# Kernel optimization log

Hardware: AMD Instinct MI355X
Metric: run time of the kernel (lower is better)

Reference implementation:

```python
import jax, jax.numpy as jnp
import numpy as np

HEADS = 8
DIM_HEAD = 64
SCALE = DIM_HEAD ** -0.5


def setup_inputs() -> dict:
    key = jax.random.key(0)
    k1, k2, k3 = jax.random.split(key, 3)
    b, dim, n = 4, 256, 2048
    hidden = HEADS * DIM_HEAD  # 512
    x = jax.random.normal(k1, (b, dim, n), dtype=jnp.float32)
    # Conv1d kernel-size-1 weights are pointwise linear maps over channels.
    w_qkv = jax.random.normal(k2, (3 * hidden, dim), dtype=jnp.float32) * (dim ** -0.5)
    w_out = jax.random.normal(k3, (dim, hidden), dtype=jnp.float32) * (hidden ** -0.5)
    b_out = jnp.zeros((dim,), dtype=jnp.float32)
    return {"x": x, "w_qkv": w_qkv, "w_out": w_out, "b_out": b_out}


def reference(x, w_qkv, w_out, b_out):
    b, dim, n = x.shape
    hidden = w_out.shape[1]
    # pointwise conv1d == channel matmul: [3h, dim] x [b, dim, n] -> [b, 3h, n]
    qkv = jnp.einsum('oi,bin->bon', w_qkv, x)
    q, k, v = jnp.split(qkv, 3, axis=1)
    # b (h c) n -> b h c n
    reshape = lambda t: t.reshape(b, HEADS, DIM_HEAD, n)
    q, k, v = reshape(q) * SCALE, reshape(k), reshape(v)
    sim = jnp.einsum('bhdi,bhdj->bhij', q, k)          # [b, h, n, n]
    attn = jax.nn.softmax(sim, axis=-1)
    out = jnp.einsum('bhij,bhdj->bhid', attn, v)        # [b, h, n, d]
    # b h n d -> b (h d) n
    out = out.transpose(0, 1, 3, 2).reshape(b, hidden, n)
    return jnp.einsum('oi,bin->bon', w_out, out) + b_out[None, :, None]
```

## Files before the change

kernel.cpp:

```cpp
#include <hip/hip_runtime.h>
#include <stdint.h>

#define SEQ  2048
#define DIMC 256
#define HID  512
#define NH   8
#define DH   64

typedef __attribute__((ext_vector_type(8))) short bf16x8;
typedef __attribute__((ext_vector_type(4))) float f32x4;
typedef __attribute__((ext_vector_type(16))) float f32x16;
typedef __attribute__((ext_vector_type(2))) unsigned uint2v;
typedef __attribute__((address_space(1))) const uint32_t guint_t;
typedef __attribute__((address_space(3))) uint32_t luint_t;

__device__ __forceinline__ void gld16(const void* g, void* l) {
  __builtin_amdgcn_global_load_lds((guint_t*)g, (luint_t*)l, 16, 0, 0);
}

__device__ __forceinline__ void barrier_raw() {
  asm volatile("" ::: "memory");
  __builtin_amdgcn_s_barrier();
  asm volatile("" ::: "memory");
}
#define WAITVM(n) asm volatile("s_waitcnt vmcnt(" #n ")" ::: "memory")

__device__ __forceinline__ unsigned short f2bf(float f) {
  union { float f; uint32_t u; } v; v.f = f;
  return (unsigned short)((v.u + 0x7FFFu + ((v.u >> 16) & 1u)) >> 16);
}

__device__ __forceinline__ uint32_t fbits(float f) {
  union { float f; uint32_t u; } v; v.f = f; return v.u;
}
__device__ __forceinline__ float ffrombits(uint32_t u) {
  union { uint32_t u; float f; } v; v.u = u; return v.f;
}

__device__ __forceinline__ uint32_t cvtpk(float a, float b) {
  uint32_t r;
  asm("v_cvt_pk_bf16_f32 %0, %1, %2" : "=v"(r) : "v"(a), "v"(b));
  return r;
}

__device__ __forceinline__ void swap32(uint32_t& a, uint32_t& b) {
#if __has_builtin(__builtin_amdgcn_permlane32_swap)
  uint2v r = __builtin_amdgcn_permlane32_swap(a, b, false, false);
  a = r[0]; b = r[1];
#else
  uint32_t aw = __shfl_xor(a, 32);
  uint32_t bw = __shfl_xor(b, 32);
  bool lo = (threadIdx.x & 32) == 0;
  uint32_t an = lo ? a : bw;
  uint32_t bn = lo ? aw : b;
  a = an; b = bn;
#endif
}

__global__ __launch_bounds__(256) void prep_kernel(
    const float* __restrict__ x, const float* __restrict__ wqkv,
    const float* __restrict__ wout,
    unsigned short* __restrict__ wqkv_b, unsigned short* __restrict__ wout_b,
    unsigned short* __restrict__ xT) {
  __shared__ float tile[64][65];
  int blk = blockIdx.x;
  int t = threadIdx.x;
  if (blk < 384) {
    int idx = blk * 1024 + t * 4;
    float4 v = *(const float4*)(wqkv + idx);
    float s = ((idx >> 8) < HID) ? 0.18033688011112042f : 1.0f;
    ushort4 o;
    o.x = f2bf(v.x * s); o.y = f2bf(v.y * s);
    o.z = f2bf(v.z * s); o.w = f2bf(v.w * s);
    *(ushort4*)(wqkv_b + idx) = o;
    return;
  }
  if (blk < 512) {
    int idx = (blk - 384) * 1024 + t * 4;
    float4 v = *(const float4*)(wout + idx);
    ushort4 o;
    o.x = f2bf(v.x); o.y = f2bf(v.y); o.z = f2bf(v.z); o.w = f2bf(v.w);
    *(ushort4*)(wout_b + idx) = o;
    return;
  }
  int tid = blk - 512;
  int b  = tid >> 7;
  int r  = tid & 127;
  int i0 = (r >> 5) * 64;
  int n0 = (r & 31) * 64;
  const float* xb = x + (size_t)b * DIMC * SEQ;
  int tn = t & 15, ti = t >> 4;
#pragma unroll
  for (int j = 0; j < 4; j++) {
    int il = ti + j * 16;
    float4 v = *(const float4*)(xb + (size_t)(i0 + il) * SEQ + n0 + tn * 4);
    tile[il][tn*4+0] = v.x; tile[il][tn*4+1] = v.y;
    tile[il][tn*4+2] = v.z; tile[il][tn*4+3] = v.w;
  }
  __syncthreads();
  unsigned short* xTb = xT + (size_t)b * SEQ * DIMC;
#pragma unroll
  for (int j = 0; j < 4; j++) {
    int nl = ti + j * 16;
    int i4 = tn * 4;
    uint2 pk;
    pk.x = (uint32_t)f2bf(tile[i4+0][nl]) | ((uint32_t)f2bf(tile[i4+1][nl]) << 16);
    pk.y = (uint32_t)f2bf(tile[i4+2][nl]) | ((uint32_t)f2bf(tile[i4+3][nl]) << 16);
    *(uint2*)(xTb + (size_t)(n0 + nl) * DIMC + i0 + i4) = pk;
  }
}

__global__ __launch_bounds__(256, 3) void qkv_gemm(
    const unsigned short* __restrict__ wq, const unsigned short* __restrict__ xT,
    unsigned short* __restrict__ Qs, unsigned short* __restrict__ Ks,
    unsigned short* __restrict__ Vt) {
  __shared__ unsigned short lds[32768];
  int id = blockIdx.x + 12 * blockIdx.y + 192 * blockIdx.z;
  int xcd = id & 7, wg = id >> 3;
  int pair = xcd * 8 + wg / 12;
  int o0 = (wg % 12) * 128;
  int n0 = (pair & 15) * 128;
  int b  = pair >> 4;
  int t  = threadIdx.x;
  int wv = t >> 6, l = t & 63, l15 = l & 15, q = l >> 4;
  int wm = (wv & 1) * 64, wn = (wv >> 1) * 64;
  f32x4 acc[4][4];
#pragma unroll
  for (int i = 0; i < 4; i++)
#pragma unroll
    for (int j = 0; j < 4; j++) acc[i][j] = (f32x4){0.f, 0.f, 0.f, 0.f};
  const unsigned short* Ag = wq + (size_t)o0 * DIMC;
  const unsigned short* Bg = xT + ((size_t)b * SEQ + n0) * DIMC;
  int lrow8 = l >> 3, lcol = l & 7;

  auto stage = [&](int kk, int buf) {
    unsigned short* la = lds + (buf << 14);
    unsigned short* lb = la + 8192;
    int k0 = kk * 64;
#pragma unroll
    for (int c0 = 0; c0 < 4; c0++) {
      int c = wv * 4 + c0;
      int row = c * 8 + lrow8;
      int sg = lcol ^ (row & 7);
      gld16(Ag + (size_t)row * DIMC + k0 + sg * 8, la + c * 512);
      gld16(Bg + (size_t)row * DIMC + k0 + sg * 8, lb + c * 512);
    }
  };

  stage(0, 0);
  for (int kk = 0; kk < 4; kk++) {
    int cur = kk & 1;
    WAITVM(0);
    barrier_raw();
    if (kk < 3) stage(kk + 1, cur ^ 1);
    unsigned short* la = lds + (cur << 14);
    unsigned short* lb = la + 8192;
#pragma unroll
    for (int kh = 0; kh < 2; kh++) {
      bf16x8 af[4], bfr[4];
#pragma unroll
      for (int mt = 0; mt < 4; mt++) {
        int row = wm + mt*16 + l15;
        af[mt] = *(const bf16x8*)(la + row*64 + ((kh*4 + q) ^ (row & 7)) * 8);
      }
#pragma unroll
      for (int nt = 0; nt < 4; nt++) {
        int row = wn + nt*16 + l15;
        bfr[nt] = *(const bf16x8*)(lb + row*64 + ((kh*4 + q) ^ (row & 7)) * 8);
      }
#pragma unroll
      for (int mt = 0; mt < 4; mt++)
#pragma unroll
        for (int nt = 0; nt < 4; nt++)
          acc[mt][nt] = __builtin_amdgcn_mfma_f32_16x16x32_bf16(af[mt], bfr[nt], acc[mt][nt], 0, 0, 0);
    }
  }
  barrier_raw();
  int seg3 = o0 >> 9;
  int h0   = (o0 & 511) >> 6;
  if (seg3 == 2) {
#pragma unroll
    for (int mt = 0; mt < 4; mt++)
#pragma unroll
      for (int nt = 0; nt < 4; nt++)
#pragma unroll
        for (int r = 0; r < 4; r++) {
          int ol = wm + mt * 16 + q * 4 + r;
          int nn = wn + nt * 16 + l15;
          lds[ol * 136 + nn] = f2bf(acc[mt][nt][r]);
        }
    __syncthreads();
#pragma unroll
    for (int i = 0; i < 8; i++) {
      int idx = i * 256 + t;
      int ol  = idx >> 4;
      int nnb = (idx & 15) * 8;
      uint4 v = *(const uint4*)(lds + ol * 136 + nnb);
      int h = h0 + (ol >> 6), d = ol & 63;
      *(uint4*)(Vt + (((size_t)b * NH + h) * DH + d) * SEQ + n0 + nnb) = v;
    }
  } else {
    unsigned short* dst = (seg3 == 0) ? Qs : Ks;
#pragma unroll
    for (int mt = 0; mt < 4; mt++)
#pragma unroll
      for (int nt = 0; nt < 4; nt++)
#pragma unroll
        for (int r = 0; r < 4; r++) {
          int ol = wm + mt * 16 + q * 4 + r;
          int nn = wn + nt * 16 + l15;
          lds[nn * 136 + ol] = f2bf(acc[mt][nt][r]);
        }
    __syncthreads();
#pragma unroll
    for (int i = 0; i < 8; i++) {
      int idx = i * 256 + t;
      int nn  = idx >> 4;
      int olb = (idx & 15) * 8;
      uint4 v = *(const uint4*)(lds + nn * 136 + olb);
      int h = h0 + (olb >> 6), d = olb & 63;
      *(uint4*)(dst + (((size_t)b * NH + h) * SEQ + n0 + nn) * DH + d) = v;
    }
  }
}

__global__ __launch_bounds__(256, 4) void attn_kernel(
    const unsigned short* __restrict__ Qs, const unsigned short* __restrict__ Ks,
    const unsigned short* __restrict__ Vt, unsigned short* __restrict__ AO) {
  __shared__ unsigned short KVs[16384];
  __shared__ float Lc[128];
  int id = blockIdx.x;
  int s  = id >> 3;
  int bh = (id & 7) * 4 + (s & 3);
  int q0 = (s >> 2) * 64;
  int b = bh >> 3, h = bh & 7;
  int t = threadIdx.x;
  int w = t >> 6, l = t & 63, l31 = l & 31, lh = l >> 5;
  int cg = w & 1, qg = w >> 1;
  const unsigned short* Qg = Qs + ((size_t)bh * SEQ + q0 + qg * 32) * DH;
  bf16x8 qb[4];
#pragma unroll
  for (int kc = 0; kc < 4; kc++)
    qb[kc] = *(const bf16x8*)(Qg + l31 * DH + kc*16 + lh*8);
  f32x16 oacc[2];
  float lsum = 0.f;
#pragma unroll
  for (int dt = 0; dt < 2; dt++)
#pragma unroll
    for (int r = 0; r < 16; r++) oacc[dt][r] = 0.f;

  const unsigned short* Ksrc = Ks + ((size_t)bh * SEQ + cg * 1024) * DH;
  const unsigned short* Vsrc = Vt + (size_t)bh * DH * SEQ + cg * 1024;

  const unsigned short* sgp[4];
  unsigned short* dst0;
  size_t step;
  if (w < 2) {
#pragma unroll
    for (int g = 0; g < 4; g++) {
      int kr = g * 8 + (l >> 3);
      sgp[g] = Ksrc + (size_t)kr * DH + ((l & 7) ^ (kr & 7)) * 8;
    }
    dst0 = (unsigned short*)KVs + cg * 2048;
    step = (size_t)32 * DH;
  } else {
#pragma unroll
    for (int g = 0; g < 4; g++) {
      int r = g * 8 + (l >> 3);
      int u = (l & 7) ^ (r & 7);
      int d = (u >> 2) * 32 + r;
      int j = u & 3;
      sgp[g] = Vsrc + (size_t)d * SEQ + j * 8;
    }
    dst0 = (unsigned short*)KVs + 4096 + cg * 2048;
    step = 32;
  }

  auto stage = [&](int it2, int buf) {
    size_t off = (size_t)it2 * step;
    unsigned short* dstb = dst0 + buf * 8192;
#pragma unroll
    for (int g = 0; g < 4; g++)
      gld16(sgp[g] + off, dstb + g * 512);
  };

  stage(0, 0);
  for (int it = 0; it < 32; it++) {
    int cur = it & 1;
    WAITVM(0);
    barrier_raw();
    if (it < 31) stage(it + 1, cur ^ 1);
    const unsigned short* Kst = KVs + cur * 8192 + cg * 2048;
    const unsigned short* Vst = KVs + cur * 8192 + 4096 + cg * 2048;
    f32x16 st;
#pragma unroll
    for (int r = 0; r < 16; r++) st[r] = 0.f;
    __builtin_amdgcn_s_setprio(1);
#pragma unroll
    for (int kc = 0; kc < 4; kc++) {
      bf16x8 kf = *(const bf16x8*)(Kst + l31 * 64 + ((kc*2 + lh) ^ (l31 & 7)) * 8);
      st = __builtin_amdgcn_mfma_f32_32x32x16_bf16(kf, qb[kc], st, 0, 0, 0);
    }
    __builtin_amdgcn_s_setprio(0);
    bf16x8 vf[2][2];
#pragma unroll
    for (int kc2 = 0; kc2 < 2; kc2++)
#pragma unroll
      for (int dt = 0; dt < 2; dt++)
        vf[kc2][dt] = *(const bf16x8*)(Vst + l31 * 64 +
                                       ((dt*4 + kc2*2 + lh) ^ (l31 & 7)) * 8);
    float p[16];
#pragma unroll
    for (int r = 0; r < 16; r++) p[r] = __builtin_amdgcn_exp2f(st[r]);
    {
      float t0 = p[0]+p[1],  t1 = p[2]+p[3],  t2 = p[4]+p[5],  t3 = p[6]+p[7];
      float t4 = p[8]+p[9],  t5 = p[10]+p[11], t6 = p[12]+p[13], t7 = p[14]+p[15];
      float u0 = t0+t1, u1 = t2+t3, u2 = t4+t5, u3 = t6+t7;
      lsum += (u0+u1) + (u2+u3);
    }
    bf16x8 af[2];
#pragma unroll
    for (int hf = 0; hf < 2; hf++) {
      uint32_t xs[4], ys[4];
#pragma unroll
      for (int j = 0; j < 4; j++) {
        xs[j] = fbits(p[hf*8 + j]);
        ys[j] = fbits(p[hf*8 + 4 + j]);
        swap32(xs[j], ys[j]);
      }
      union { uint32_t u[4]; bf16x8 v; } cv;
      cv.u[0] = cvtpk(ffrombits(xs[0]), ffrombits(xs[1]));
      cv.u[1] = cvtpk(ffrombits(xs[2]), ffrombits(xs[3]));
      cv.u[2] = cvtpk(ffrombits(ys[0]), ffrombits(ys[1]));
      cv.u[3] = cvtpk(ffrombits(ys[2]), ffrombits(ys[3]));
      af[hf] = cv.v;
    }
    __builtin_amdgcn_s_setprio(1);
#pragma unroll
    for (int kc2 = 0; kc2 < 2; kc2++)
#pragma unroll
      for (int dt = 0; dt < 2; dt++)
        oacc[dt] = __builtin_amdgcn_mfma_f32_32x32x16_bf16(af[kc2], vf[kc2][dt], oacc[dt], 0, 0, 0);
    __builtin_amdgcn_s_setprio(0);
  }
  {
    float v = lsum;
    v += __shfl_xor(v, 32);
    if (l < 32) Lc[cg * 64 + qg * 32 + l31] = v;
  }
  __syncthreads();
  float* Oc = (float*)KVs;
  if (cg == 1) {
#pragma unroll
    for (int dt = 0; dt < 2; dt++)
#pragma unroll
      for (int r = 0; r < 16; r++) {
        int qrow = qg*32 + (r & 3) + 8*(r >> 2) + 4*lh;
        Oc[qrow * 64 + dt*32 + l31] = oacc[dt][r];
      }
  }
  __syncthreads();
  if (cg == 0) {
    unsigned short* AOb = AO + (size_t)b * SEQ * HID + h * DH;
#pragma unroll
    for (int r = 0; r < 16; r++) {
      int qrow = qg*32 + (r & 3) + 8*(r >> 2) + 4*lh;
      float inv = __builtin_amdgcn_rcpf(Lc[qrow] + Lc[64 + qrow]);
      int n = q0 + qrow;
#pragma unroll
      for (int dt = 0; dt < 2; dt++) {
        float val = (oacc[dt][r] + Oc[qrow * 64 + dt*32 + l31]) * inv;
        AOb[(size_t)n * HID + dt*32 + l31] = f2bf(val);
      }
    }
  }
}

__global__ __launch_bounds__(256, 2) void out_gemm(
    const unsigned short* __restrict__ wo, const unsigned short* __restrict__ AO,
    const float* __restrict__ bias, float* __restrict__ out) {
  __shared__ unsigned short lds[16384];
  int id = blockIdx.x + 4 * blockIdx.y + 128 * blockIdx.z;
  int xcd = id & 7, wg = id >> 3;
  int pair = xcd * 16 + (wg >> 2);
  int o0 = (wg & 3) * 64;
  int n0 = (pair & 31) * 64;
  int b  = pair >> 5;
  int t  = threadIdx.x;
  int wv = t >> 6, l = t & 63, l15 = l & 15, q = l >> 4;
  int wm = (wv & 1) * 32, wn = (wv >> 1) * 32;
  f32x4 acc[2][2];
#pragma unroll
  for (int i = 0; i < 2; i++)
#pragma unroll
    for (int j = 0; j < 2; j++) acc[i][j] = (f32x4){0.f,0.f,0.f,0.f};
  const unsigned short* Ag = wo + (size_t)o0 * HID;
  const unsigned short* Bg = AO + ((size_t)b * SEQ + n0) * HID;
  int lrow8 = l >> 3, lcol = l & 7;

  auto stage = [&](int kk, int buf) {
    unsigned short* la = lds + buf * 8192;
    unsigned short* lb = la + 4096;
    int k0 = kk * 64;
#pragma unroll
    for (int c0 = 0; c0 < 2; c0++) {
      int c = wv * 2 + c0;
      int row = c * 8 + lrow8;
      int sg = lcol ^ (row & 7);
      gld16(Ag + (size_t)row * HID + k0 + sg * 8, la + c * 512);
      gld16(Bg + (size_t)row * HID + k0 + sg * 8, lb + c * 512);
    }
  };

  stage(0, 0);
  for (int kk = 0; kk < 8; kk++) {
    int cur = kk & 1;
    WAITVM(0);
    barrier_raw();
    if (kk < 7) stage(kk + 1, cur ^ 1);
    unsigned short* la = lds + cur * 8192;
    unsigned short* lb = la + 4096;
#pragma unroll
    for (int kh = 0; kh < 2; kh++) {
      bf16x8 af[2], bfr[2];
#pragma unroll
      for (int mt = 0; mt < 2; mt++) {
        int row = wm + mt*16 + l15;
        af[mt] = *(const bf16x8*)(la + row*64 + ((kh*4 + q) ^ (row & 7)) * 8);
      }
#pragma unroll
      for (int nt = 0; nt < 2; nt++) {
        int row = wn + nt*16 + l15;
        bfr[nt] = *(const bf16x8*)(lb + row*64 + ((kh*4 + q) ^ (row & 7)) * 8);
      }
#pragma unroll
      for (int mt = 0; mt < 2; mt++)
#pragma unroll
        for (int nt = 0; nt < 2; nt++)
          acc[mt][nt] = __builtin_amdgcn_mfma_f32_16x16x32_bf16(af[mt], bfr[nt], acc[mt][nt], 0,0,0);
    }
  }
#pragma unroll
  for (int mt = 0; mt < 2; mt++)
#pragma unroll
    for (int nt = 0; nt < 2; nt++)
#pragma unroll
      for (int r = 0; r < 4; r++) {
        int o2 = o0 + wm + mt*16 + q*4 + r;
        int n  = n0 + wn + nt*16 + l15;
        out[((size_t)b * DIMC + o2) * SEQ + n] = acc[mt][nt][r] + bias[o2];
      }
}

extern "C" void kernel_launch(void* const* d_in, const int* in_sizes, int n_in,
                              void* d_out, int out_size, void* d_ws, size_t ws_size,
                              hipStream_t stream) {
  const float* x    = (const float*)d_in[0];
  const float* wqkv = (const float*)d_in[1];
  const float* wout = (const float*)d_in[2];
  const float* bout = (const float*)d_in[3];
  float* out = (float*)d_out;
  char* ws = (char*)d_ws;
  unsigned short* wqkv_b = (unsigned short*)(ws);
  unsigned short* wout_b = (unsigned short*)(ws + 786432);
  unsigned short* xT     = (unsigned short*)(ws + 1048576);
  unsigned short* Qs     = (unsigned short*)(ws + 5242880);
  unsigned short* Ks     = (unsigned short*)(ws + 13631488);
  unsigned short* Vt     = (unsigned short*)(ws + 22020096);
  unsigned short* AO     = (unsigned short*)(ws + 30408704);
  prep_kernel<<<1024, 256, 0, stream>>>(x, wqkv, wout, wqkv_b, wout_b, xT);
  qkv_gemm<<<dim3(12, 16, 4), 256, 0, stream>>>(wqkv_b, xT, Qs, Ks, Vt);
  attn_kernel<<<1024, 256, 0, stream>>>(Qs, Ks, Vt, AO);
  out_gemm<<<dim3(4, 32, 4), 256, 0, stream>>>(wout_b, AO, bout, out);
}
```

Before: 137.3 us.

## Split attention keys across four waves with per-wave private K/V pipelines

Each wave now handles all 64 query rows (two 32-row tiles) over its own quarter of the key sequence, so each K fragment read from LDS feeds two MFMAs. Each wave stages its own K and V tiles into private double buffers using vmcnt-based waits instead of block-wide barriers inside the loop. The four partial outputs and row sums are reduced through LDS at the end. LDS per block doubles and launch bounds drop to 2 blocks per SU, which lowers occupancy and adds a larger final reduction.

Result: slower. 144.7 us (+5.4%).

```diff
diff --git a/kernel.cpp b/kernel.cpp
--- a/kernel.cpp
+++ b/kernel.cpp
@@ -224,11 +224,11 @@
   }
 }
 
-__global__ __launch_bounds__(256, 4) void attn_kernel(
+__global__ __launch_bounds__(256, 2) void attn_kernel(
     const unsigned short* __restrict__ Qs, const unsigned short* __restrict__ Ks,
     const unsigned short* __restrict__ Vt, unsigned short* __restrict__ AO) {
-  __shared__ unsigned short KVs[16384];
-  __shared__ float Lc[128];
+  __shared__ unsigned short KVs[32768];
+  __shared__ float Lc[256];
   int id = blockIdx.x;
   int s  = id >> 3;
   int bh = (id & 7) * 4 + (s & 3);
@@ -236,70 +236,62 @@
   int b = bh >> 3, h = bh & 7;
   int t = threadIdx.x;
   int w = t >> 6, l = t & 63, l31 = l & 31, lh = l >> 5;
-  int cg = w & 1, qg = w >> 1;
-  const unsigned short* Qg = Qs + ((size_t)bh * SEQ + q0 + qg * 32) * DH;
-  bf16x8 qb[4];
-#pragma unroll
-  for (int kc = 0; kc < 4; kc++)
-    qb[kc] = *(const bf16x8*)(Qg + l31 * DH + kc*16 + lh*8);
-  f32x16 oacc[2];
-  float lsum = 0.f;
-#pragma unroll
-  for (int dt = 0; dt < 2; dt++)
-#pragma unroll
-    for (int r = 0; r < 16; r++) oacc[dt][r] = 0.f;
-
-  const unsigned short* Ksrc = Ks + ((size_t)bh * SEQ + cg * 1024) * DH;
-  const unsigned short* Vsrc = Vt + (size_t)bh * DH * SEQ + cg * 1024;
-
-  const unsigned short* sgp[4];
-  unsigned short* dst0;
-  size_t step;
-  if (w < 2) {
+
+  const unsigned short* Qg = Qs + ((size_t)bh * SEQ + q0) * DH;
+  bf16x8 qb[2][4];
+#pragma unroll
+  for (int qt = 0; qt < 2; qt++)
+#pragma unroll
+    for (int kc = 0; kc < 4; kc++)
+      qb[qt][kc] = *(const bf16x8*)(Qg + (qt*32 + l31) * DH + kc*16 + lh*8);
+
+  f32x16 oacc[2][2];
+  float lsum0 = 0.f, lsum1 = 0.f;
+#pragma unroll
+  for (int qt = 0; qt < 2; qt++)
+#pragma unroll
+    for (int dt = 0; dt < 2; dt++)
+#pragma unroll
+      for (int r = 0; r < 16; r++) oacc[qt][dt][r] = 0.f;
+
+  const unsigned short* Ksrc = Ks + ((size_t)bh * SEQ + w * 512) * DH;
+  const unsigned short* Vsrc = Vt + (size_t)bh * DH * SEQ + w * 512;
+  int l3 = l >> 3, l7 = l & 7;
+  int u  = l7 ^ (l3 & 7);
+  const unsigned short* Kg0 = Ksrc + (size_t)l3 * DH + u * 8;
+  const unsigned short* Vg0 = Vsrc + (size_t)((u >> 2) * 32 + l3) * SEQ + (u & 3) * 8;
+  unsigned short* myK = (unsigned short*)KVs + w * 8192;
+
+  auto stage = [&](int it2, int buf) {
+    const unsigned short* kp = Kg0 + (size_t)it2 * 32 * DH;
+    const unsigned short* vp = Vg0 + it2 * 32;
+    unsigned short* kd = myK + buf * 4096;
+    unsigned short* vd = kd + 2048;
 #pragma unroll
     for (int g = 0; g < 4; g++) {
-      int kr = g * 8 + (l >> 3);
-      sgp[g] = Ksrc + (size_t)kr * DH + ((l & 7) ^ (kr & 7)) * 8;
-    }
-    dst0 = (unsigned short*)KVs + cg * 2048;
-    step = (size_t)32 * DH;
-  } else {
-#pragma unroll
-    for (int g = 0; g < 4; g++) {
-      int r = g * 8 + (l >> 3);
-      int u = (l & 7) ^ (r & 7);
-      int d = (u >> 2) * 32 + r;
-      int j = u & 3;
-      sgp[g] = Vsrc + (size_t)d * SEQ + j * 8;
-    }
-    dst0 = (unsigned short*)KVs + 4096 + cg * 2048;
-    step = 32;
-  }
-
-  auto stage = [&](int it2, int buf) {
-    size_t off = (size_t)it2 * step;
-    unsigned short* dstb = dst0 + buf * 8192;
-#pragma unroll
-    for (int g = 0; g < 4; g++)
-      gld16(sgp[g] + off, dstb + g * 512);
+      gld16(kp + g * 8 * DH, kd + g * 512);
+      gld16(vp + (size_t)g * 8 * SEQ, vd + g * 512);
+    }
   };
 
   stage(0, 0);
-  for (int it = 0; it < 32; it++) {
-    int cur = it & 1;
-    WAITVM(0);
-    barrier_raw();
-    if (it < 31) stage(it + 1, cur ^ 1);
-    const unsigned short* Kst = KVs + cur * 8192 + cg * 2048;
-    const unsigned short* Vst = KVs + cur * 8192 + 4096 + cg * 2048;
-    f32x16 st;
-#pragma unroll
-    for (int r = 0; r < 16; r++) st[r] = 0.f;
+  stage(1, 1);
+  for (int it = 0; it < 16; it++) {
+    int buf = it & 1;
+    if (it == 15) { WAITVM(0); } else { WAITVM(8); }
+    const unsigned short* Kst = myK + buf * 4096;
+    const unsigned short* Vst = Kst + 2048;
+    f32x16 st[2];
+#pragma unroll
+    for (int qt = 0; qt < 2; qt++)
+#pragma unroll
+      for (int r = 0; r < 16; r++) st[qt][r] = 0.f;
     __builtin_amdgcn_s_setprio(1);
 #pragma unroll
     for (int kc = 0; kc < 4; kc++) {
       bf16x8 kf = *(const bf16x8*)(Kst + l31 * 64 + ((kc*2 + lh) ^ (l31 & 7)) * 8);
-      st = __builtin_amdgcn_mfma_f32_32x32x16_bf16(kf, qb[kc], st, 0, 0, 0);
+      st[0] = __builtin_amdgcn_mfma_f32_32x32x16_bf16(kf, qb[0][kc], st[0], 0, 0, 0);
+      st[1] = __builtin_amdgcn_mfma_f32_32x32x16_bf16(kf, qb[1][kc], st[1], 0, 0, 0);
     }
     __builtin_amdgcn_s_setprio(0);
     bf16x8 vf[2][2];
@@ -309,70 +301,82 @@
       for (int dt = 0; dt < 2; dt++)
         vf[kc2][dt] = *(const bf16x8*)(Vst + l31 * 64 +
                                        ((dt*4 + kc2*2 + lh) ^ (l31 & 7)) * 8);
-    float p[16];
-#pragma unroll
-    for (int r = 0; r < 16; r++) p[r] = __builtin_amdgcn_exp2f(st[r]);
-    {
-      float t0 = p[0]+p[1],  t1 = p[2]+p[3],  t2 = p[4]+p[5],  t3 = p[6]+p[7];
-      float t4 = p[8]+p[9],  t5 = p[10]+p[11], t6 = p[12]+p[13], t7 = p[14]+p[15];
-      float u0 = t0+t1, u1 = t2+t3, u2 = t4+t5, u3 = t6+t7;
-      lsum += (u0+u1) + (u2+u3);
-    }
-    bf16x8 af[2];
-#pragma unroll
-    for (int hf = 0; hf < 2; hf++) {
-      uint32_t xs[4], ys[4];
-#pragma unroll
-      for (int j = 0; j < 4; j++) {
-        xs[j] = fbits(p[hf*8 + j]);
-        ys[j] = fbits(p[hf*8 + 4 + j]);
-        swap32(xs[j], ys[j]);
-      }
-      union { uint32_t u[4]; bf16x8 v; } cv;
-      cv.u[0] = cvtpk(ffrombits(xs[0]), ffrombits(xs[1]));
-      cv.u[1] = cvtpk(ffrombits(xs[2]), ffrombits(xs[3]));
-      cv.u[2] = cvtpk(ffrombits(ys[0]), ffrombits(ys[1]));
-      cv.u[3] = cvtpk(ffrombits(ys[2]), ffrombits(ys[3]));
-      af[hf] = cv.v;
-    }
-    __builtin_amdgcn_s_setprio(1);
-#pragma unroll
-    for (int kc2 = 0; kc2 < 2; kc2++)
+#pragma unroll
+    for (int qt = 0; qt < 2; qt++) {
+      float p[16];
+#pragma unroll
+      for (int r = 0; r < 16; r++) p[r] = __builtin_amdgcn_exp2f(st[qt][r]);
+      {
+        float t0=p[0]+p[1],  t1=p[2]+p[3],  t2=p[4]+p[5],   t3=p[6]+p[7];
+        float t4=p[8]+p[9],  t5=p[10]+p[11], t6=p[12]+p[13], t7=p[14]+p[15];
+        float a = ((t0+t1)+(t2+t3)) + ((t4+t5)+(t6+t7));
+        if (qt == 0) lsum0 += a; else lsum1 += a;
+      }
+      bf16x8 af[2];
+#pragma unroll
+      for (int hf = 0; hf < 2; hf++) {
+        uint32_t xs[4], ys[4];
+#pragma unroll
+        for (int j = 0; j < 4; j++) {
+          xs[j] = fbits(p[hf*8 + j]);
+          ys[j] = fbits(p[hf*8 + 4 + j]);
+          swap32(xs[j], ys[j]);
+        }
+        union { uint32_t u[4]; bf16x8 v; } cv;
+        cv.u[0] = cvtpk(ffrombits(xs[0]), ffrombits(xs[1]));
+        cv.u[1] = cvtpk(ffrombits(xs[2]), ffrombits(xs[3]));
+        cv.u[2] = cvtpk(ffrombits(ys[0]), ffrombits(ys[1]));
+        cv.u[3] = cvtpk(ffrombits(ys[2]), ffrombits(ys[3]));
+        af[hf] = cv.v;
+      }
+      __builtin_amdgcn_s_setprio(1);
+#pragma unroll
+      for (int kc2 = 0; kc2 < 2; kc2++)
+#pragma unroll
+        for (int dt = 0; dt < 2; dt++)
+          oacc[qt][dt] = __builtin_amdgcn_mfma_f32_32x32x16_bf16(af[kc2], vf[kc2][dt], oacc[qt][dt], 0, 0, 0);
+      __builtin_amdgcn_s_setprio(0);
+    }
+    if (it < 14) {
+      asm volatile("s_waitcnt lgkmcnt(0)" ::: "memory");
+      stage(it + 2, buf);
+    }
+  }
+  lsum0 += __shfl_xor(lsum0, 32);
+  lsum1 += __shfl_xor(lsum1, 32);
+  if (l < 32) { Lc[w*64 + l31] = lsum0; Lc[w*64 + 32 + l31] = lsum1; }
+  __syncthreads();
+  float* Ob = (float*)KVs;
+  if (w > 0) {
+    float* Ow = Ob + (w - 1) * 4096;
+#pragma unroll
+    for (int qt = 0; qt < 2; qt++)
 #pragma unroll
       for (int dt = 0; dt < 2; dt++)
-        oacc[dt] = __builtin_amdgcn_mfma_f32_32x32x16_bf16(af[kc2], vf[kc2][dt], oacc[dt], 0, 0, 0);
-    __builtin_amdgcn_s_setprio(0);
-  }
-  {
-    float v = lsum;
-    v += __shfl_xor(v, 32);
-    if (l < 32) Lc[cg * 64 + qg * 32 + l31] = v;
+#pragma unroll
+        for (int r = 0; r < 16; r++) {
+          int qrow = qt*32 + (r & 3) + 8*(r >> 2) + 4*lh;
+          Ow[qrow * 64 + dt*32 + l31] = oacc[qt][dt][r];
+        }
   }
   __syncthreads();
-  float* Oc = (float*)KVs;
-  if (cg == 1) {
-#pragma unroll
-    for (int dt = 0; dt < 2; dt++)
+  if (w == 0) {
+    unsigned short* AOb = AO + (size_t)b * SEQ * HID + h * DH;
+#pragma unroll
+    for (int qt = 0; qt < 2; qt++)
 #pragma unroll
       for (int r = 0; r < 16; r++) {
-        int qrow = qg*32 + (r & 3) + 8*(r >> 2) + 4*lh;
-        Oc[qrow * 64 + dt*32 + l31] = oacc[dt][r];
-      }
-  }
-  __syncthreads();
-  if (cg == 0) {
-    unsigned short* AOb = AO + (size_t)b * SEQ * HID + h * DH;
-#pragma unroll
-    for (int r = 0; r < 16; r++) {
-      int qrow = qg*32 + (r & 3) + 8*(r >> 2) + 4*lh;
-      float inv = __builtin_amdgcn_rcpf(Lc[qrow] + Lc[64 + qrow]);
-      int n = q0 + qrow;
-#pragma unroll
-      for (int dt = 0; dt < 2; dt++) {
-        float val = (oacc[dt][r] + Oc[qrow * 64 + dt*32 + l31]) * inv;
-        AOb[(size_t)n * HID + dt*32 + l31] = f2bf(val);
-      }
-    }
+        int qrow = qt*32 + (r & 3) + 8*(r >> 2) + 4*lh;
+        float inv = __builtin_amdgcn_rcpf(Lc[qrow] + Lc[64 + qrow] +
+                                          Lc[128 + qrow] + Lc[192 + qrow]);
+        int n = q0 + qrow;
+#pragma unroll
+        for (int dt = 0; dt < 2; dt++) {
+          int idx = qrow * 64 + dt*32 + l31;
+          float val = (oacc[qt][dt][r] + Ob[idx] + Ob[4096 + idx] + Ob[8192 + idx]) * inv;
+          AOb[(size_t)n * HID + dt*32 + l31] = f2bf(val);
+        }
+      }
   }
 }
 
```

## Double attention query tile per block so more waves share K/V staging

Applied to the files above, without the earlier changes.

The attention kernel now runs 512-thread blocks, each covering 128 queries instead of 64, with half as many blocks. Each staged K/V tile in LDS is reused by four query groups instead of two, which halves global K/V traffic per query. The load work is split across eight waves, and the row-sum and partial-output reduction buffers are resized. The launch bound of 512 threads with 4 blocks per CU caps per-thread registers more tightly, which could cause spills. Only 512 blocks are launched, so the grid fills the device less evenly.

Measured after the change: 130.1 us. -5.2%, faster.

```diff
diff --git a/kernel.cpp b/kernel.cpp
--- a/kernel.cpp
+++ b/kernel.cpp
@@ -224,15 +224,15 @@
   }
 }
 
-__global__ __launch_bounds__(256, 4) void attn_kernel(
+__global__ __launch_bounds__(512, 4) void attn_kernel(
     const unsigned short* __restrict__ Qs, const unsigned short* __restrict__ Ks,
     const unsigned short* __restrict__ Vt, unsigned short* __restrict__ AO) {
   __shared__ unsigned short KVs[16384];
-  __shared__ float Lc[128];
+  __shared__ float Lc[256];
   int id = blockIdx.x;
   int s  = id >> 3;
   int bh = (id & 7) * 4 + (s & 3);
-  int q0 = (s >> 2) * 64;
+  int q0 = (s >> 2) * 128;
   int b = bh >> 3, h = bh & 7;
   int t = threadIdx.x;
   int w = t >> 6, l = t & 63, l31 = l & 31, lh = l >> 5;
@@ -249,39 +249,40 @@
 #pragma unroll
     for (int r = 0; r < 16; r++) oacc[dt][r] = 0.f;
 
-  const unsigned short* Ksrc = Ks + ((size_t)bh * SEQ + cg * 1024) * DH;
-  const unsigned short* Vsrc = Vt + (size_t)bh * DH * SEQ + cg * 1024;
-
-  const unsigned short* sgp[4];
+  int which = w >> 1, half = w & 1;
+  const unsigned short* sgp[2];
   unsigned short* dst0;
   size_t step;
-  if (w < 2) {
-#pragma unroll
-    for (int g = 0; g < 4; g++) {
+  if (which < 2) {
+    const unsigned short* Ksrc = Ks + ((size_t)bh * SEQ + which * 1024) * DH;
+#pragma unroll
+    for (int gi = 0; gi < 2; gi++) {
+      int g = half * 2 + gi;
       int kr = g * 8 + (l >> 3);
-      sgp[g] = Ksrc + (size_t)kr * DH + ((l & 7) ^ (kr & 7)) * 8;
-    }
-    dst0 = (unsigned short*)KVs + cg * 2048;
+      sgp[gi] = Ksrc + (size_t)kr * DH + ((l & 7) ^ (kr & 7)) * 8;
+    }
+    dst0 = (unsigned short*)KVs + which * 2048 + half * 1024;
     step = (size_t)32 * DH;
   } else {
-#pragma unroll
-    for (int g = 0; g < 4; g++) {
+    const unsigned short* Vsrc = Vt + (size_t)bh * DH * SEQ + (which - 2) * 1024;
+#pragma unroll
+    for (int gi = 0; gi < 2; gi++) {
+      int g = half * 2 + gi;
       int r = g * 8 + (l >> 3);
       int u = (l & 7) ^ (r & 7);
       int d = (u >> 2) * 32 + r;
       int j = u & 3;
-      sgp[g] = Vsrc + (size_t)d * SEQ + j * 8;
-    }
-    dst0 = (unsigned short*)KVs + 4096 + cg * 2048;
+      sgp[gi] = Vsrc + (size_t)d * SEQ + j * 8;
+    }
+    dst0 = (unsigned short*)KVs + 4096 + (which - 2) * 2048 + half * 1024;
     step = 32;
   }
 
   auto stage = [&](int it2, int buf) {
     size_t off = (size_t)it2 * step;
     unsigned short* dstb = dst0 + buf * 8192;
-#pragma unroll
-    for (int g = 0; g < 4; g++)
-      gld16(sgp[g] + off, dstb + g * 512);
+    gld16(sgp[0] + off, dstb);
+    gld16(sgp[1] + off, dstb + 512);
   };
 
   stage(0, 0);
@@ -313,10 +314,9 @@
 #pragma unroll
     for (int r = 0; r < 16; r++) p[r] = __builtin_amdgcn_exp2f(st[r]);
     {
-      float t0 = p[0]+p[1],  t1 = p[2]+p[3],  t2 = p[4]+p[5],  t3 = p[6]+p[7];
-      float t4 = p[8]+p[9],  t5 = p[10]+p[11], t6 = p[12]+p[13], t7 = p[14]+p[15];
-      float u0 = t0+t1, u1 = t2+t3, u2 = t4+t5, u3 = t6+t7;
-      lsum += (u0+u1) + (u2+u3);
+      float t0=p[0]+p[1],  t1=p[2]+p[3],  t2=p[4]+p[5],   t3=p[6]+p[7];
+      float t4=p[8]+p[9],  t5=p[10]+p[11], t6=p[12]+p[13], t7=p[14]+p[15];
+      lsum += ((t0+t1)+(t2+t3)) + ((t4+t5)+(t6+t7));
     }
     bf16x8 af[2];
 #pragma unroll
@@ -346,7 +346,7 @@
   {
     float v = lsum;
     v += __shfl_xor(v, 32);
-    if (l < 32) Lc[cg * 64 + qg * 32 + l31] = v;
+    if (l < 32) Lc[cg * 128 + qg * 32 + l31] = v;
   }
   __syncthreads();
   float* Oc = (float*)KVs;
@@ -365,7 +365,7 @@
 #pragma unroll
     for (int r = 0; r < 16; r++) {
       int qrow = qg*32 + (r & 3) + 8*(r >> 2) + 4*lh;
-      float inv = __builtin_amdgcn_rcpf(Lc[qrow] + Lc[64 + qrow]);
+      float inv = __builtin_amdgcn_rcpf(Lc[qrow] + Lc[128 + qrow]);
       int n = q0 + qrow;
 #pragma unroll
       for (int dt = 0; dt < 2; dt++) {
@@ -470,6 +470,6 @@
   unsigned short* AO     = (unsigned short*)(ws + 30408704);
   prep_kernel<<<1024, 256, 0, stream>>>(x, wqkv, wout, wqkv_b, wout_b, xT);
   qkv_gemm<<<dim3(12, 16, 4), 256, 0, stream>>>(wqkv_b, xT, Qs, Ks, Vt);
-  attn_kernel<<<1024, 256, 0, stream>>>(Qs, Ks, Vt, AO);
+  attn_kernel<<<512, 512, 0, stream>>>(Qs, Ks, Vt, AO);
   out_gemm<<<dim3(4, 32, 4), 256, 0, stream>>>(wout_b, AO, bout, out);
 }
```
